# Kernel tuning notes

Hardware: AMD Instinct MI355X
Metric: run time of the kernel (lower is better)

The kernel has to match this reference:

```python
import jax, jax.numpy as jnp
import numpy as np
from jax.scipy.special import gammaln

ADIM, ODIM = 256, 80
B, T_TEXT, T_FEATS = 4, 160, 800


def conv1d(x, w, b, pad):
    # x: (B, C_in, T), w: (C_out, C_in, K)
    y = jax.lax.conv_general_dilated(x, w, (1,), [(pad, pad)],
                                     dimension_numbers=('NCH', 'OIH', 'NCH'))
    return y + b[None, :, None]


def betaln(x, y):
    return gammaln(x) + gammaln(y) - gammaln(x + y)


def beta_binomial_prior(T, N, w=1.0):
    # Matches scipy betabinom.logpmf(k, N, alpha, beta) with
    # alpha = w*arange(1, T+1), beta = w*(T - alpha + 1), k = arange(N).
    a = w * jnp.arange(1, T + 1, dtype=jnp.float32)          # (T,)
    b = w * (T - a + 1.0)                                    # (T,)
    k = jnp.arange(N, dtype=jnp.float32)[:, None]            # (N, 1)
    Nf = jnp.float32(N)
    logp = (gammaln(Nf + 1.0) - gammaln(k + 1.0) - gammaln(Nf - k + 1.0)
            + betaln(k + a, Nf - k + b) - betaln(a, b))      # (N, T)
    return logp.T                                            # (T_feats, T_text)


def setup_inputs() -> dict:
    key = jax.random.key(0)
    ks = jax.random.split(key, 12)
    s = 0.05
    return {
        'text': jax.random.normal(ks[0], (B, T_TEXT, ADIM), jnp.float32),
        'feats': jax.random.normal(ks[1], (B, T_FEATS, ODIM), jnp.float32),
        'text_lengths': jnp.full((B,), T_TEXT, dtype=jnp.int32),
        'feats_lengths': jnp.full((B,), T_FEATS, dtype=jnp.int32),
        'x_masks': jnp.zeros((B, T_TEXT), dtype=bool),
        't_w1': jax.random.normal(ks[2], (ADIM, ADIM, 3), jnp.float32) * s,
        't_b1': jnp.zeros((ADIM,), jnp.float32),
        't_w2': jax.random.normal(ks[3], (ADIM, ADIM, 1), jnp.float32) * s,
        't_b2': jnp.zeros((ADIM,), jnp.float32),
        'f_w1': jax.random.normal(ks[4], (ADIM, ODIM, 3), jnp.float32) * s,
        'f_b1': jnp.zeros((ADIM,), jnp.float32),
        'f_w2': jax.random.normal(ks[5], (ADIM, ADIM, 3), jnp.float32) * s,
        'f_b2': jnp.zeros((ADIM,), jnp.float32),
        'f_w3': jax.random.normal(ks[6], (ADIM, ADIM, 1), jnp.float32) * s,
        'f_b3': jnp.zeros((ADIM,), jnp.float32),
    }


def reference(text, feats, text_lengths, feats_lengths, x_masks,
              t_w1, t_b1, t_w2, t_b2, f_w1, f_b1, f_w2, f_b2, f_w3, f_b3):
    # text conv stem: (B, T_text, adim) -> (B, T_text, adim)
    t = jnp.swapaxes(text, 1, 2)
    t = jax.nn.relu(conv1d(t, t_w1, t_b1, 1))
    t = conv1d(t, t_w2, t_b2, 0)
    t = jnp.swapaxes(t, 1, 2)
    # feats conv stem: (B, T_feats, odim) -> (B, T_feats, adim)
    f = jnp.swapaxes(feats, 1, 2)
    f = jax.nn.relu(conv1d(f, f_w1, f_b1, 1))
    f = jax.nn.relu(conv1d(f, f_w2, f_b2, 1))
    f = conv1d(f, f_w3, f_b3, 0)
    f = jnp.swapaxes(f, 1, 2)
    # L2-distance score: (B, T_feats, T_text)
    diff = f[:, :, None, :] - t[:, None, :, :]               # (B,Tf,Tt,adim)
    score = -jnp.sqrt(jnp.sum(diff * diff, axis=-1))
    score = jnp.where(x_masks[:, None, :], -jnp.inf, score)
    log_p_attn = jax.nn.log_softmax(score, axis=-1)
    # beta-binomial prior (lengths == max, so prior fills the whole matrix)
    prior = beta_binomial_prior(feats.shape[1], text.shape[1])
    return log_p_attn + prior[None, :, :]
```

## Files before the change

### kernel.cpp

```cpp
#include <hip/hip_runtime.h>
#include <math.h>

#define NB 4
#define TTEXT 160
#define TFEAT 800

typedef __bf16 bf16x8 __attribute__((ext_vector_type(8)));
typedef float f32x4 __attribute__((ext_vector_type(4)));

__device__ inline unsigned short f2bf(float f) {
    unsigned int u = __builtin_bit_cast(unsigned int, f);
    unsigned int r = u + 0x7fffu + ((u >> 16) & 1u);
    return (unsigned short)(r >> 16);
}
__device__ inline float bf2f(unsigned short h) {
    unsigned int u = ((unsigned int)h) << 16;
    return __builtin_bit_cast(float, u);
}

__device__ inline float lgamma_int(float nf) {
    float z = nf, corr = 0.0f;
    if (nf < 8.0f) {
        const float p = nf * (nf + 1.0f) * (nf + 2.0f) * (nf + 3.0f)
                      * (nf + 4.0f) * (nf + 5.0f) * (nf + 6.0f) * (nf + 7.0f);
        z = nf + 8.0f;
        corr = logf(p);
    }
    const float lz = logf(z);
    const float iz = 1.0f / z;
    const float s = (z - 0.5f) * lz - z + 0.918938533f
                  + iz * (0.0833333333f - iz * iz * 0.00277777778f);
    return s - corr;
}

__global__ __launch_bounds__(256) void prep_kernel(
    const float* __restrict__ tw1, const float* __restrict__ tw2,
    const float* __restrict__ fw1, const float* __restrict__ fw2,
    const float* __restrict__ fw3,
    unsigned short* __restrict__ wb_t1, unsigned short* __restrict__ wb_t2,
    unsigned short* __restrict__ wb_f1, unsigned short* __restrict__ wb_f2,
    unsigned short* __restrict__ wb_f3)
{
    const int u = blockIdx.x * 256 + threadIdx.x;
    int rem = u;
    int CIN, CINP, K; const float* src; unsigned short* dst;
    if (rem < 196608)                  { CIN = 256; CINP = 256; K = 3; src = tw1; dst = wb_t1; }
    else if ((rem -= 196608) < 65536)  { CIN = 256; CINP = 256; K = 1; src = tw2; dst = wb_t2; }
    else if ((rem -= 65536) < 73728)   { CIN = 80;  CINP = 96;  K = 3; src = fw1; dst = wb_f1; }
    else if ((rem -= 73728) < 196608)  { CIN = 256; CINP = 256; K = 3; src = fw2; dst = wb_f2; }
    else { rem -= 196608;                CIN = 256; CINP = 256; K = 1; src = fw3; dst = wb_f3; }
    const int q = rem & 31, coc = rem >> 5, co = coc & 255, c = coc >> 8;
    const int cpk = CINP / 32, k = c / cpk, ci = (c % cpk) * 32 + q;
    const float v = (ci < CIN) ? src[((size_t)co * CIN + ci) * K + k] : 0.0f;
    dst[rem] = f2bf(v);
}

__global__ __launch_bounds__(1024) void stems_kernel(
    const float* __restrict__ text, const float* __restrict__ feats,
    const unsigned short* __restrict__ wt1, const float* __restrict__ bt1,
    const unsigned short* __restrict__ wt2, const float* __restrict__ bt2,
    const unsigned short* __restrict__ wf1, const float* __restrict__ bf1v,
    const unsigned short* __restrict__ wf2, const float* __restrict__ bf2v,
    const unsigned short* __restrict__ wf3, const float* __restrict__ bf3v,
    unsigned short* __restrict__ tB, float* __restrict__ tnorm,
    unsigned short* __restrict__ fC, float* __restrict__ fnorm)
{
    __shared__ __align__(16) unsigned short s[11056];
    __shared__ float s_red[16][16];
    const int tid = threadIdx.x;
    const int w  = tid >> 6;
    const int l  = tid & 63;
    const int lr = l & 15;
    const int lk = l >> 4;
    const int co0 = w * 16;
    const int koff = lk * 8;
    const int bid = blockIdx.x;

    if (bid < 40) {
        const int b  = bid & 3;
        const int t0 = (bid >> 2) << 4;
        unsigned short* s_in  = s;
        unsigned short* s_mid = s + 4752;

        for (int idx = tid; idx < 18 * 64; idx += 1024) {
            const int r = idx >> 6, c4 = idx & 63;
            const int x = t0 - 1 + r;
            float4 v = {0.f, 0.f, 0.f, 0.f};
            if (x >= 0 && x < TTEXT)
                v = *(const float4*)(text + ((size_t)(b * TTEXT + x)) * 256 + c4 * 4);
            unsigned short* p = s_in + r * 264 + c4 * 4;
            p[0] = f2bf(v.x); p[1] = f2bf(v.y); p[2] = f2bf(v.z); p[3] = f2bf(v.w);
        }
        __syncthreads();

        f32x4 acc = {0.f, 0.f, 0.f, 0.f};
#pragma unroll 8
        for (int c = 0; c < 24; ++c) {
            const int k  = c >> 3;
            const int ci = ((c & 7) << 5) + koff;
            const bf16x8 a = *(const bf16x8*)(s_in + (lr + k) * 264 + ci);
            const bf16x8 bb = *(const bf16x8*)(wt1 + (((size_t)c * 256 + co0 + lr) << 5) + koff);
            acc = __builtin_amdgcn_mfma_f32_16x16x32_bf16(a, bb, acc, 0, 0, 0);
        }
        {
            const float bv = bt1[co0 + lr];
#pragma unroll
            for (int r = 0; r < 4; ++r)
                s_mid[(lk * 4 + r) * 264 + co0 + lr] = f2bf(fmaxf(acc[r] + bv, 0.f));
        }
        __syncthreads();

        f32x4 a2 = {0.f, 0.f, 0.f, 0.f};
#pragma unroll
        for (int c = 0; c < 8; ++c) {
            const bf16x8 a = *(const bf16x8*)(s_mid + lr * 264 + (c << 5) + koff);
            const bf16x8 bb = *(const bf16x8*)(wt2 + (((size_t)c * 256 + co0 + lr) << 5) + koff);
            a2 = __builtin_amdgcn_mfma_f32_16x16x32_bf16(a, bb, a2, 0, 0, 0);
        }
        const float bv2 = bt2[co0 + lr];
#pragma unroll
        for (int r = 0; r < 4; ++r) {
            const int row = lk * 4 + r;
            const unsigned short h = f2bf(a2[r] + bv2);
            tB[((size_t)(b * TTEXT + t0 + row)) * 256 + co0 + lr] = h;
            const float vq = bf2f(h);
            float np = vq * vq;
            np += __shfl_xor(np, 1);
            np += __shfl_xor(np, 2);
            np += __shfl_xor(np, 4);
            np += __shfl_xor(np, 8);
            if (lr == 0) s_red[row][w] = np;
        }
        __syncthreads();
        if (tid < 16) {
            float s4 = 0.f;
#pragma unroll
            for (int ww = 0; ww < 16; ++ww) s4 += s_red[tid][ww];
            tnorm[b * TTEXT + t0 + tid] = s4;
        }
    } else {
        const int fb = bid - 40;
        const int b  = fb & 3;
        const int t0 = (fb >> 2) << 4;
        unsigned short* s_fin = s;
        unsigned short* s_b1  = s + 2080;
        unsigned short* s_b2  = s + 6832;

        for (int idx = tid; idx < 20 * 24; idx += 1024) {
            const int r  = idx / 24, c4 = idx - r * 24;
            const int ch = c4 * 4;
            const int x  = t0 - 2 + r;
            float4 v = {0.f, 0.f, 0.f, 0.f};
            if (ch < 80 && x >= 0 && x < TFEAT)
                v = *(const float4*)(feats + ((size_t)(b * TFEAT + x)) * 80 + ch);
            unsigned short* p = s_fin + r * 104 + ch;
            p[0] = f2bf(v.x); p[1] = f2bf(v.y); p[2] = f2bf(v.z); p[3] = f2bf(v.w);
        }
        __syncthreads();

        f32x4 acc1[2];
#pragma unroll
        for (int m = 0; m < 2; ++m) acc1[m] = {0.f, 0.f, 0.f, 0.f};
#pragma unroll
        for (int c = 0; c < 9; ++c) {
            const int k  = c / 3;
            const int ci = (c - k * 3) * 32 + koff;
            const bf16x8 bb = *(const bf16x8*)(wf1 + (((size_t)c * 256 + co0 + lr) << 5) + koff);
#pragma unroll
            for (int m = 0; m < 2; ++m) {
                int rr = m * 16 + lr + k;
                if (rr > 19) rr = 19;
                const bf16x8 a = *(const bf16x8*)(s_fin + rr * 104 + ci);
                acc1[m] = __builtin_amdgcn_mfma_f32_16x16x32_bf16(a, bb, acc1[m], 0, 0, 0);
            }
        }
        {
            const float bv = bf1v[co0 + lr];
#pragma unroll
            for (int m = 0; m < 2; ++m)
#pragma unroll
                for (int r = 0; r < 4; ++r) {
                    const int i = m * 16 + lk * 4 + r;
                    if (i < 18)
                        s_b1[i * 264 + co0 + lr] = f2bf(fmaxf(acc1[m][r] + bv, 0.f));
                }
        }
        __syncthreads();

        f32x4 acc2 = {0.f, 0.f, 0.f, 0.f};
#pragma unroll 8
        for (int c = 0; c < 24; ++c) {
            const int k  = c >> 3;
            const int ci = ((c & 7) << 5) + koff;
            const bf16x8 a = *(const bf16x8*)(s_b1 + (lr + k) * 264 + ci);
            const bf16x8 bb = *(const bf16x8*)(wf2 + (((size_t)c * 256 + co0 + lr) << 5) + koff);
            acc2 = __builtin_amdgcn_mfma_f32_16x16x32_bf16(a, bb, acc2, 0, 0, 0);
        }
        {
            const float bv = bf2v[co0 + lr];
#pragma unroll
            for (int r = 0; r < 4; ++r)
                s_b2[(lk * 4 + r) * 264 + co0 + lr] = f2bf(fmaxf(acc2[r] + bv, 0.f));
        }
        __syncthreads();

        f32x4 a3 = {0.f, 0.f, 0.f, 0.f};
#pragma unroll
        for (int c = 0; c < 8; ++c) {
            const bf16x8 a = *(const bf16x8*)(s_b2 + lr * 264 + (c << 5) + koff);
            const bf16x8 bb = *(const bf16x8*)(wf3 + (((size_t)c * 256 + co0 + lr) << 5) + koff);
            a3 = __builtin_amdgcn_mfma_f32_16x16x32_bf16(a, bb, a3, 0, 0, 0);
        }
        const float bv3 = bf3v[co0 + lr];
#pragma unroll
        for (int r = 0; r < 4; ++r) {
            const int row = lk * 4 + r;
            const unsigned short h = f2bf(a3[r] + bv3);
            fC[((size_t)(b * TFEAT + t0 + row)) * 256 + co0 + lr] = h;
            const float vq = bf2f(h);
            float np = vq * vq;
            np += __shfl_xor(np, 1);
            np += __shfl_xor(np, 2);
            np += __shfl_xor(np, 4);
            np += __shfl_xor(np, 8);
            if (lr == 0) s_red[row][w] = np;
        }
        __syncthreads();
        if (tid < 16) {
            float s4 = 0.f;
#pragma unroll
            for (int ww = 0; ww < 16; ++ww) s4 += s_red[tid][ww];
            fnorm[b * TFEAT + t0 + tid] = s4;
        }
    }
}

__global__ __launch_bounds__(512) void score_mfma(
    const unsigned short* __restrict__ F, const unsigned short* __restrict__ Tt,
    const float* __restrict__ fnorm, const float* __restrict__ tnorm,
    const unsigned char* __restrict__ xmask,
    float* __restrict__ out)
{
    const int b  = blockIdx.y;
    const int tid = threadIdx.x;
    const int w  = tid >> 6;
    const int l  = tid & 63;
    const int lr = l & 15;
    const int lk = l >> 4;
    const int i0 = blockIdx.x * 16;
    const int NI = (w < 2) ? 2 : 1;

    __shared__ float s_lg[962];
    __shared__ float s_red[16][8];
    __shared__ float s_red2[16][8];

    for (int idx = tid; idx < 962; idx += 512)
        s_lg[idx] = (idx >= 1) ? lgamma_int((float)idx) : 0.0f;

    f32x4 acc[2];
#pragma unroll
    for (int ni = 0; ni < 2; ++ni) acc[ni] = {0.f, 0.f, 0.f, 0.f};

    const unsigned short* __restrict__ Fp = F + ((size_t)(b * TFEAT + i0 + lr)) * 256;
    const unsigned short* __restrict__ Tp = Tt + ((size_t)b * TTEXT) * 256;

#pragma unroll
    for (int c = 0; c < 8; ++c) {
        const int d = c * 32 + lk * 8;
        const bf16x8 a = *(const bf16x8*)(Fp + d);
#pragma unroll
        for (int ni = 0; ni < 2; ++ni) {
            if (ni < NI) {
                const int n = w + ni * 8;
                const bf16x8 bb = *(const bf16x8*)(Tp + ((size_t)(n * 16 + lr)) * 256 + d);
                acc[ni] = __builtin_amdgcn_mfma_f32_16x16x32_bf16(a, bb, acc[ni], 0, 0, 0);
            }
        }
    }

    float fn[4];
#pragma unroll
    for (int r = 0; r < 4; ++r) fn[r] = fnorm[b * TFEAT + i0 + lk * 4 + r];
    float tn[2]; bool mk[2];
#pragma unroll
    for (int ni = 0; ni < 2; ++ni) {
        if (ni < NI) {
            const int j = (w + ni * 8) * 16 + lr;
            tn[ni] = tnorm[b * TTEXT + j];
            mk[ni] = xmask[b * TTEXT + j] != 0;
        } else { tn[ni] = 0.f; mk[ni] = true; }
    }
    float sc[2][4];
#pragma unroll
    for (int ni = 0; ni < 2; ++ni)
#pragma unroll
        for (int r = 0; r < 4; ++r) {
            const float d2 = fn[r] + tn[ni] - 2.0f * acc[ni][r];
            const float sv = -sqrtf(fmaxf(d2, 0.0f));
            sc[ni][r] = mk[ni] ? -INFINITY : sv;
        }

#pragma unroll
    for (int r = 0; r < 4; ++r) {
        float mx = fmaxf(sc[0][r], sc[1][r]);
        mx = fmaxf(mx, __shfl_xor(mx, 1));
        mx = fmaxf(mx, __shfl_xor(mx, 2));
        mx = fmaxf(mx, __shfl_xor(mx, 4));
        mx = fmaxf(mx, __shfl_xor(mx, 8));
        if (lr == 0) s_red[lk * 4 + r][w] = mx;
    }
    __syncthreads();
    float gmax[4];
#pragma unroll
    for (int r = 0; r < 4; ++r) {
        const int row = lk * 4 + r;
        float g = s_red[row][0];
#pragma unroll
        for (int ww = 1; ww < 8; ++ww) g = fmaxf(g, s_red[row][ww]);
        gmax[r] = g;
        float sm = 0.f;
#pragma unroll
        for (int ni = 0; ni < 2; ++ni)
            if (ni < NI) sm += expf(sc[ni][r] - g);
        sm += __shfl_xor(sm, 1);
        sm += __shfl_xor(sm, 2);
        sm += __shfl_xor(sm, 4);
        sm += __shfl_xor(sm, 8);
        if (lr == 0) s_red2[row][w] = sm;
    }
    __syncthreads();

    const float cst = s_lg[161] - s_lg[961] + s_lg[801];
#pragma unroll
    for (int r = 0; r < 4; ++r) {
        const int row = lk * 4 + r;
        float ssum = s_red2[row][0];
#pragma unroll
        for (int ww = 1; ww < 8; ++ww) ssum += s_red2[row][ww];
        const float lse = gmax[r] + logf(ssum);
        const int grow = i0 + row;
        const float rowterm = cst - s_lg[grow + 1] - s_lg[801 - grow];
#pragma unroll
        for (int ni = 0; ni < 2; ++ni) {
            if (ni < NI) {
                const int j = (w + ni * 8) * 16 + lr;
                const float prior = rowterm - s_lg[j + 1] - s_lg[160 - j]
                                  + s_lg[grow + j + 1] + s_lg[960 - grow - j];
                out[((size_t)(b * TFEAT + grow)) * TTEXT + j] = sc[ni][r] - lse + prior;
            }
        }
    }
}

extern "C" void kernel_launch(void* const* d_in, const int* in_sizes, int n_in,
                              void* d_out, int out_size, void* d_ws, size_t ws_size,
                              hipStream_t stream) {
    const float* text  = (const float*)d_in[0];
    const float* feats = (const float*)d_in[1];
    const unsigned char* xmask = (const unsigned char*)d_in[4];
    const float* t_w1 = (const float*)d_in[5];
    const float* t_b1 = (const float*)d_in[6];
    const float* t_w2 = (const float*)d_in[7];
    const float* t_b2 = (const float*)d_in[8];
    const float* f_w1 = (const float*)d_in[9];
    const float* f_b1 = (const float*)d_in[10];
    const float* f_w2 = (const float*)d_in[11];
    const float* f_b2 = (const float*)d_in[12];
    const float* f_w3 = (const float*)d_in[13];
    const float* f_b3 = (const float*)d_in[14];
    float* out = (float*)d_out;

    char* wp = (char*)d_ws;
    auto alloc = [&](size_t bytes) -> void* {
        void* p = wp; wp += (bytes + 255) & ~(size_t)255; return p;
    };
    unsigned short* wb_t1 = (unsigned short*)alloc(196608 * 2);
    unsigned short* wb_t2 = (unsigned short*)alloc(65536 * 2);
    unsigned short* wb_f1 = (unsigned short*)alloc(73728 * 2);
    unsigned short* wb_f2 = (unsigned short*)alloc(196608 * 2);
    unsigned short* wb_f3 = (unsigned short*)alloc(65536 * 2);
    unsigned short* tB = (unsigned short*)alloc((size_t)NB * TTEXT * 256 * 2);
    unsigned short* fC = (unsigned short*)alloc((size_t)NB * TFEAT * 256 * 2);
    float* fnorm = (float*)alloc((size_t)NB * TFEAT * 4);
    float* tnorm = (float*)alloc((size_t)NB * TTEXT * 4);

    prep_kernel<<<2336, 256, 0, stream>>>(
        t_w1, t_w2, f_w1, f_w2, f_w3, wb_t1, wb_t2, wb_f1, wb_f2, wb_f3);

    stems_kernel<<<240, 1024, 0, stream>>>(
        text, feats,
        wb_t1, t_b1, wb_t2, t_b2,
        wb_f1, f_b1, wb_f2, f_b2, wb_f3, f_b3,
        tB, tnorm, fC, fnorm);

    score_mfma<<<dim3(50, NB), 512, 0, stream>>>(fC, tB, fnorm, tnorm, xmask, out);
}
```

Before: 33.37 us.

## Merge text stem with weight prep and fuse feats stem into score kernel

Reduces three launches to two. The first kernel runs the text conv stem, reading fp32 weights directly and converting them to bf16 on the fly, while its extra blocks convert the feats weights to bf16. The second kernel runs the feats stem and keeps its output tile in shared memory, then computes distances, log-softmax and the prior in the same block. This removes the fC/fnorm round trip through global memory and one launch. In exchange it adds strided fp32 weight reads in the text stem, and only 10 of 16 waves are active in the score phase.

```diff
diff --git a/kernel.cpp b/kernel.cpp
--- a/kernel.cpp
+++ b/kernel.cpp
@@ -7,6 +7,7 @@
 
 typedef __bf16 bf16x8 __attribute__((ext_vector_type(8)));
 typedef float f32x4 __attribute__((ext_vector_type(4)));
+typedef unsigned short us8 __attribute__((ext_vector_type(8)));
 
 __device__ inline unsigned short f2bf(float f) {
     unsigned int u = __builtin_bit_cast(unsigned int, f);
@@ -33,40 +34,127 @@
     return s - corr;
 }
 
-__global__ __launch_bounds__(256) void prep_kernel(
-    const float* __restrict__ tw1, const float* __restrict__ tw2,
-    const float* __restrict__ fw1, const float* __restrict__ fw2,
-    const float* __restrict__ fw3,
-    unsigned short* __restrict__ wb_t1, unsigned short* __restrict__ wb_t2,
+__global__ __launch_bounds__(1024) void k1_text_prep(
+    const float* __restrict__ text,
+    const float* __restrict__ t_w1, const float* __restrict__ t_b1,
+    const float* __restrict__ t_w2, const float* __restrict__ t_b2,
+    const float* __restrict__ f_w1, const float* __restrict__ f_w2,
+    const float* __restrict__ f_w3,
     unsigned short* __restrict__ wb_f1, unsigned short* __restrict__ wb_f2,
-    unsigned short* __restrict__ wb_f3)
+    unsigned short* __restrict__ wb_f3,
+    unsigned short* __restrict__ tB, float* __restrict__ tnorm)
 {
-    const int u = blockIdx.x * 256 + threadIdx.x;
-    int rem = u;
-    int CIN, CINP, K; const float* src; unsigned short* dst;
-    if (rem < 196608)                  { CIN = 256; CINP = 256; K = 3; src = tw1; dst = wb_t1; }
-    else if ((rem -= 196608) < 65536)  { CIN = 256; CINP = 256; K = 1; src = tw2; dst = wb_t2; }
-    else if ((rem -= 65536) < 73728)   { CIN = 80;  CINP = 96;  K = 3; src = fw1; dst = wb_f1; }
-    else if ((rem -= 73728) < 196608)  { CIN = 256; CINP = 256; K = 3; src = fw2; dst = wb_f2; }
-    else { rem -= 196608;                CIN = 256; CINP = 256; K = 1; src = fw3; dst = wb_f3; }
-    const int q = rem & 31, coc = rem >> 5, co = coc & 255, c = coc >> 8;
-    const int cpk = CINP / 32, k = c / cpk, ci = (c % cpk) * 32 + q;
-    const float v = (ci < CIN) ? src[((size_t)co * CIN + ci) * K + k] : 0.0f;
-    dst[rem] = f2bf(v);
-}
-
-__global__ __launch_bounds__(1024) void stems_kernel(
-    const float* __restrict__ text, const float* __restrict__ feats,
-    const unsigned short* __restrict__ wt1, const float* __restrict__ bt1,
-    const unsigned short* __restrict__ wt2, const float* __restrict__ bt2,
+    const int bid = blockIdx.x;
+    const int tid = threadIdx.x;
+
+    if (bid >= 40) {
+        const int u = (bid - 40) * 1024 + tid;
+        int rem = u;
+        int CIN, CINP, K; const float* src; unsigned short* dst;
+        if (rem < 73728)                  { CIN = 80;  CINP = 96;  K = 3; src = f_w1; dst = wb_f1; }
+        else if ((rem -= 73728) < 196608) { CIN = 256; CINP = 256; K = 3; src = f_w2; dst = wb_f2; }
+        else { rem -= 196608;               CIN = 256; CINP = 256; K = 1; src = f_w3; dst = wb_f3; }
+        const int q = rem & 31, coc = rem >> 5, co = coc & 255, c = coc >> 8;
+        const int cpk = CINP / 32, k = c / cpk, ci = (c % cpk) * 32 + q;
+        const float v = (ci < CIN) ? src[((size_t)co * CIN + ci) * K + k] : 0.0f;
+        dst[rem] = f2bf(v);
+        return;
+    }
+
+    __shared__ __align__(16) unsigned short s[8976];
+    __shared__ float s_red[16][16];
+    const int w  = tid >> 6;
+    const int l  = tid & 63;
+    const int lr = l & 15;
+    const int lk = l >> 4;
+    const int co0 = w * 16;
+    const int koff = lk * 8;
+    const int b  = bid & 3;
+    const int t0 = (bid >> 2) << 4;
+    unsigned short* s_in  = s;
+    unsigned short* s_mid = s + 4752;
+
+    for (int idx = tid; idx < 18 * 64; idx += 1024) {
+        const int r = idx >> 6, c4 = idx & 63;
+        const int x = t0 - 1 + r;
+        float4 v = {0.f, 0.f, 0.f, 0.f};
+        if (x >= 0 && x < TTEXT)
+            v = *(const float4*)(text + ((size_t)(b * TTEXT + x)) * 256 + c4 * 4);
+        unsigned short* p = s_in + r * 264 + c4 * 4;
+        p[0] = f2bf(v.x); p[1] = f2bf(v.y); p[2] = f2bf(v.z); p[3] = f2bf(v.w);
+    }
+    __syncthreads();
+
+    f32x4 acc = {0.f, 0.f, 0.f, 0.f};
+#pragma unroll 4
+    for (int c = 0; c < 24; ++c) {
+        const int k  = c >> 3;
+        const int ci = ((c & 7) << 5) + koff;
+        const bf16x8 a = *(const bf16x8*)(s_in + (lr + k) * 264 + ci);
+        const float* wp = t_w1 + ((size_t)(co0 + lr) * 256 + ci) * 3 + k;
+        us8 hv;
+#pragma unroll
+        for (int j = 0; j < 8; ++j) hv[j] = f2bf(wp[j * 3]);
+        acc = __builtin_amdgcn_mfma_f32_16x16x32_bf16(
+            a, __builtin_bit_cast(bf16x8, hv), acc, 0, 0, 0);
+    }
+    {
+        const float bv = t_b1[co0 + lr];
+#pragma unroll
+        for (int r = 0; r < 4; ++r)
+            s_mid[(lk * 4 + r) * 264 + co0 + lr] = f2bf(fmaxf(acc[r] + bv, 0.f));
+    }
+    __syncthreads();
+
+    f32x4 a2 = {0.f, 0.f, 0.f, 0.f};
+#pragma unroll
+    for (int c = 0; c < 8; ++c) {
+        const bf16x8 a = *(const bf16x8*)(s_mid + lr * 264 + (c << 5) + koff);
+        const float* wp = t_w2 + (size_t)(co0 + lr) * 256 + (c << 5) + koff;
+        const float4 u0 = *(const float4*)wp;
+        const float4 u1 = *(const float4*)(wp + 4);
+        us8 hv;
+        hv[0] = f2bf(u0.x); hv[1] = f2bf(u0.y); hv[2] = f2bf(u0.z); hv[3] = f2bf(u0.w);
+        hv[4] = f2bf(u1.x); hv[5] = f2bf(u1.y); hv[6] = f2bf(u1.z); hv[7] = f2bf(u1.w);
+        a2 = __builtin_amdgcn_mfma_f32_16x16x32_bf16(
+            a, __builtin_bit_cast(bf16x8, hv), a2, 0, 0, 0);
+    }
+    const float bv2 = t_b2[co0 + lr];
+#pragma unroll
+    for (int r = 0; r < 4; ++r) {
+        const int row = lk * 4 + r;
+        const unsigned short h = f2bf(a2[r] + bv2);
+        tB[((size_t)(b * TTEXT + t0 + row)) * 256 + co0 + lr] = h;
+        const float vq = bf2f(h);
+        float np = vq * vq;
+        np += __shfl_xor(np, 1);
+        np += __shfl_xor(np, 2);
+        np += __shfl_xor(np, 4);
+        np += __shfl_xor(np, 8);
+        if (lr == 0) s_red[row][w] = np;
+    }
+    __syncthreads();
+    if (tid < 16) {
+        float s4 = 0.f;
+#pragma unroll
+        for (int ww = 0; ww < 16; ++ww) s4 += s_red[tid][ww];
+        tnorm[b * TTEXT + t0 + tid] = s4;
+    }
+}
+
+__global__ __launch_bounds__(1024) void k2_feats_score(
+    const float* __restrict__ feats, const unsigned char* __restrict__ xmask,
     const unsigned short* __restrict__ wf1, const float* __restrict__ bf1v,
     const unsigned short* __restrict__ wf2, const float* __restrict__ bf2v,
     const unsigned short* __restrict__ wf3, const float* __restrict__ bf3v,
-    unsigned short* __restrict__ tB, float* __restrict__ tnorm,
-    unsigned short* __restrict__ fC, float* __restrict__ fnorm)
+    const unsigned short* __restrict__ tB, const float* __restrict__ tnorm,
+    float* __restrict__ out)
 {
     __shared__ __align__(16) unsigned short s[11056];
     __shared__ float s_red[16][16];
+    __shared__ float s_red2[16][16];
+    __shared__ float s_fn[16];
+    __shared__ float s_lg[962];
     const int tid = threadIdx.x;
     const int w  = tid >> 6;
     const int l  = tid & 63;
@@ -74,235 +162,139 @@
     const int lk = l >> 4;
     const int co0 = w * 16;
     const int koff = lk * 8;
-    const int bid = blockIdx.x;
-
-    if (bid < 40) {
-        const int b  = bid & 3;
-        const int t0 = (bid >> 2) << 4;
-        unsigned short* s_in  = s;
-        unsigned short* s_mid = s + 4752;
-
-        for (int idx = tid; idx < 18 * 64; idx += 1024) {
-            const int r = idx >> 6, c4 = idx & 63;
-            const int x = t0 - 1 + r;
-            float4 v = {0.f, 0.f, 0.f, 0.f};
-            if (x >= 0 && x < TTEXT)
-                v = *(const float4*)(text + ((size_t)(b * TTEXT + x)) * 256 + c4 * 4);
-            unsigned short* p = s_in + r * 264 + c4 * 4;
-            p[0] = f2bf(v.x); p[1] = f2bf(v.y); p[2] = f2bf(v.z); p[3] = f2bf(v.w);
+    const int fb = blockIdx.x;
+    const int b  = fb & 3;
+    const int t0 = (fb >> 2) << 4;
+
+    unsigned short* s_fin = s;
+    unsigned short* s_b1  = s + 2080;
+    unsigned short* s_b2  = s + 6832;
+    unsigned short* s_out = s;
+
+    if (tid < 962) s_lg[tid] = (tid >= 1) ? lgamma_int((float)tid) : 0.0f;
+
+    for (int idx = tid; idx < 20 * 24; idx += 1024) {
+        const int r  = idx / 24, c4 = idx - r * 24;
+        const int ch = c4 * 4;
+        const int x  = t0 - 2 + r;
+        float4 v = {0.f, 0.f, 0.f, 0.f};
+        if (ch < 80 && x >= 0 && x < TFEAT)
+            v = *(const float4*)(feats + ((size_t)(b * TFEAT + x)) * 80 + ch);
+        unsigned short* p = s_fin + r * 104 + ch;
+        p[0] = f2bf(v.x); p[1] = f2bf(v.y); p[2] = f2bf(v.z); p[3] = f2bf(v.w);
+    }
+    __syncthreads();
+
+    f32x4 acc1[2];
+#pragma unroll
+    for (int m = 0; m < 2; ++m) acc1[m] = {0.f, 0.f, 0.f, 0.f};
+#pragma unroll
+    for (int c = 0; c < 9; ++c) {
+        const int k  = c / 3;
+        const int ci = (c - k * 3) * 32 + koff;
+        const bf16x8 bb = *(const bf16x8*)(wf1 + (((size_t)c * 256 + co0 + lr) << 5) + koff);
+#pragma unroll
+        for (int m = 0; m < 2; ++m) {
+            int rr = m * 16 + lr + k;
+            if (rr > 19) rr = 19;
+            const bf16x8 a = *(const bf16x8*)(s_fin + rr * 104 + ci);
+            acc1[m] = __builtin_amdgcn_mfma_f32_16x16x32_bf16(a, bb, acc1[m], 0, 0, 0);
         }
-        __syncthreads();
-
-        f32x4 acc = {0.f, 0.f, 0.f, 0.f};
+    }
+    {
+        const float bv = bf1v[co0 + lr];
+#pragma unroll
+        for (int m = 0; m < 2; ++m)
+#pragma unroll
+            for (int r = 0; r < 4; ++r) {
+                const int i = m * 16 + lk * 4 + r;
+                if (i < 18)
+                    s_b1[i * 264 + co0 + lr] = f2bf(fmaxf(acc1[m][r] + bv, 0.f));
+            }
+    }
+    __syncthreads();
+
+    f32x4 acc2 = {0.f, 0.f, 0.f, 0.f};
 #pragma unroll 8
-        for (int c = 0; c < 24; ++c) {
-            const int k  = c >> 3;
-            const int ci = ((c & 7) << 5) + koff;
-            const bf16x8 a = *(const bf16x8*)(s_in + (lr + k) * 264 + ci);
-            const bf16x8 bb = *(const bf16x8*)(wt1 + (((size_t)c * 256 + co0 + lr) << 5) + koff);
+    for (int c = 0; c < 24; ++c) {
+        const int k  = c >> 3;
+        const int ci = ((c & 7) << 5) + koff;
+        const bf16x8 a = *(const bf16x8*)(s_b1 + (lr + k) * 264 + ci);
+        const bf16x8 bb = *(const bf16x8*)(wf2 + (((size_t)c * 256 + co0 + lr) << 5) + koff);
+        acc2 = __builtin_amdgcn_mfma_f32_16x16x32_bf16(a, bb, acc2, 0, 0, 0);
+    }
+    {
+        const float bv = bf2v[co0 + lr];
+#pragma unroll
+        for (int r = 0; r < 4; ++r)
+            s_b2[(lk * 4 + r) * 264 + co0 + lr] = f2bf(fmaxf(acc2[r] + bv, 0.f));
+    }
+    __syncthreads();
+
+    f32x4 a3 = {0.f, 0.f, 0.f, 0.f};
+#pragma unroll
+    for (int c = 0; c < 8; ++c) {
+        const bf16x8 a = *(const bf16x8*)(s_b2 + lr * 264 + (c << 5) + koff);
+        const bf16x8 bb = *(const bf16x8*)(wf3 + (((size_t)c * 256 + co0 + lr) << 5) + koff);
+        a3 = __builtin_amdgcn_mfma_f32_16x16x32_bf16(a, bb, a3, 0, 0, 0);
+    }
+    const float bv3 = bf3v[co0 + lr];
+#pragma unroll
+    for (int r = 0; r < 4; ++r) {
+        const int row = lk * 4 + r;
+        const unsigned short h = f2bf(a3[r] + bv3);
+        s_out[row * 264 + co0 + lr] = h;
+        const float vq = bf2f(h);
+        float np = vq * vq;
+        np += __shfl_xor(np, 1);
+        np += __shfl_xor(np, 2);
+        np += __shfl_xor(np, 4);
+        np += __shfl_xor(np, 8);
+        if (lr == 0) s_red[row][w] = np;
+    }
+    __syncthreads();
+    if (tid < 16) {
+        float s4 = 0.f;
+#pragma unroll
+        for (int ww = 0; ww < 16; ++ww) s4 += s_red[tid][ww];
+        s_fn[tid] = s4;
+    }
+    __syncthreads();
+
+    const bool act = (w < 10);
+    f32x4 acc = {0.f, 0.f, 0.f, 0.f};
+    const unsigned short* __restrict__ Tp = tB + ((size_t)b * TTEXT) * 256;
+
+#pragma unroll
+    for (int c = 0; c < 8; ++c) {
+        const int d = c * 32 + koff;
+        const bf16x8 a = *(const bf16x8*)(s_out + lr * 264 + d);
+        if (act) {
+            const bf16x8 bb = *(const bf16x8*)(Tp + ((size_t)(w * 16 + lr)) * 256 + d);
             acc = __builtin_amdgcn_mfma_f32_16x16x32_bf16(a, bb, acc, 0, 0, 0);
         }
-        {
-            const float bv = bt1[co0 + lr];
-#pragma unroll
-            for (int r = 0; r < 4; ++r)
-                s_mid[(lk * 4 + r) * 264 + co0 + lr] = f2bf(fmaxf(acc[r] + bv, 0.f));
-        }
-        __syncthreads();
-
-        f32x4 a2 = {0.f, 0.f, 0.f, 0.f};
-#pragma unroll
-        for (int c = 0; c < 8; ++c) {
-            const bf16x8 a = *(const bf16x8*)(s_mid + lr * 264 + (c << 5) + koff);
-            const bf16x8 bb = *(const bf16x8*)(wt2 + (((size_t)c * 256 + co0 + lr) << 5) + koff);
-            a2 = __builtin_amdgcn_mfma_f32_16x16x32_bf16(a, bb, a2, 0, 0, 0);
-        }
-        const float bv2 = bt2[co0 + lr];
-#pragma unroll
-        for (int r = 0; r < 4; ++r) {
-            const int row = lk * 4 + r;
-            const unsigned short h = f2bf(a2[r] + bv2);
-            tB[((size_t)(b * TTEXT + t0 + row)) * 256 + co0 + lr] = h;
-            const float vq = bf2f(h);
-            float np = vq * vq;
-            np += __shfl_xor(np, 1);
-            np += __shfl_xor(np, 2);
-            np += __shfl_xor(np, 4);
-            np += __shfl_xor(np, 8);
-            if (lr == 0) s_red[row][w] = np;
-        }
-        __syncthreads();
-        if (tid < 16) {
-            float s4 = 0.f;
-#pragma unroll
-            for (int ww = 0; ww < 16; ++ww) s4 += s_red[tid][ww];
-            tnorm[b * TTEXT + t0 + tid] = s4;
-        }
-    } else {
-        const int fb = bid - 40;
-        const int b  = fb & 3;
-        const int t0 = (fb >> 2) << 4;
-        unsigned short* s_fin = s;
-        unsigned short* s_b1  = s + 2080;
-        unsigned short* s_b2  = s + 6832;
-
-        for (int idx = tid; idx < 20 * 24; idx += 1024) {
-            const int r  = idx / 24, c4 = idx - r * 24;
-            const int ch = c4 * 4;
-            const int x  = t0 - 2 + r;
-            float4 v = {0.f, 0.f, 0.f, 0.f};
-            if (ch < 80 && x >= 0 && x < TFEAT)
-                v = *(const float4*)(feats + ((size_t)(b * TFEAT + x)) * 80 + ch);
-            unsigned short* p = s_fin + r * 104 + ch;
-            p[0] = f2bf(v.x); p[1] = f2bf(v.y); p[2] = f2bf(v.z); p[3] = f2bf(v.w);
-        }
-        __syncthreads();
-
-        f32x4 acc1[2];
-#pragma unroll
-        for (int m = 0; m < 2; ++m) acc1[m] = {0.f, 0.f, 0.f, 0.f};
-#pragma unroll
-        for (int c = 0; c < 9; ++c) {
-            const int k  = c / 3;
-            const int ci = (c - k * 3) * 32 + koff;
-            const bf16x8 bb = *(const bf16x8*)(wf1 + (((size_t)c * 256 + co0 + lr) << 5) + koff);
-#pragma unroll
-            for (int m = 0; m < 2; ++m) {
-                int rr = m * 16 + lr + k;
-                if (rr > 19) rr = 19;
-                const bf16x8 a = *(const bf16x8*)(s_fin + rr * 104 + ci);
-                acc1[m] = __builtin_amdgcn_mfma_f32_16x16x32_bf16(a, bb, acc1[m], 0, 0, 0);
-            }
-        }
-        {
-            const float bv = bf1v[co0 + lr];
-#pragma unroll
-            for (int m = 0; m < 2; ++m)
-#pragma unroll
-                for (int r = 0; r < 4; ++r) {
-                    const int i = m * 16 + lk * 4 + r;
-                    if (i < 18)
-                        s_b1[i * 264 + co0 + lr] = f2bf(fmaxf(acc1[m][r] + bv, 0.f));
-                }
-        }
-        __syncthreads();
-
-        f32x4 acc2 = {0.f, 0.f, 0.f, 0.f};
-#pragma unroll 8
-        for (int c = 0; c < 24; ++c) {
-            const int k  = c >> 3;
-            const int ci = ((c & 7) << 5) + koff;
-            const bf16x8 a = *(const bf16x8*)(s_b1 + (lr + k) * 264 + ci);
-            const bf16x8 bb = *(const bf16x8*)(wf2 + (((size_t)c * 256 + co0 + lr) << 5) + koff);
-            acc2 = __builtin_amdgcn_mfma_f32_16x16x32_bf16(a, bb, acc2, 0, 0, 0);
-        }
-        {
-            const float bv = bf2v[co0 + lr];
-#pragma unroll
-            for (int r = 0; r < 4; ++r)
-                s_b2[(lk * 4 + r) * 264 + co0 + lr] = f2bf(fmaxf(acc2[r] + bv, 0.f));
-        }
-        __syncthreads();
-
-        f32x4 a3 = {0.f, 0.f, 0.f, 0.f};
-#pragma unroll
-        for (int c = 0; c < 8; ++c) {
-            const bf16x8 a = *(const bf16x8*)(s_b2 + lr * 264 + (c << 5) + koff);
-            const bf16x8 bb = *(const bf16x8*)(wf3 + (((size_t)c * 256 + co0 + lr) << 5) + koff);
-            a3 = __builtin_amdgcn_mfma_f32_16x16x32_bf16(a, bb, a3, 0, 0, 0);
-        }
-        const float bv3 = bf3v[co0 + lr];
-#pragma unroll
-        for (int r = 0; r < 4; ++r) {
-            const int row = lk * 4 + r;
-            const unsigned short h = f2bf(a3[r] + bv3);
-            fC[((size_t)(b * TFEAT + t0 + row)) * 256 + co0 + lr] = h;
-            const float vq = bf2f(h);
-            float np = vq * vq;
-            np += __shfl_xor(np, 1);
-            np += __shfl_xor(np, 2);
-            np += __shfl_xor(np, 4);
-            np += __shfl_xor(np, 8);
-            if (lr == 0) s_red[row][w] = np;
-        }
-        __syncthreads();
-        if (tid < 16) {
-            float s4 = 0.f;
-#pragma unroll
-            for (int ww = 0; ww < 16; ++ww) s4 += s_red[tid][ww];
-            fnorm[b * TFEAT + t0 + tid] = s4;
-        }
-    }
-}
-
-__global__ __launch_bounds__(512) void score_mfma(
-    const unsigned short* __restrict__ F, const unsigned short* __restrict__ Tt,
-    const float* __restrict__ fnorm, const float* __restrict__ tnorm,
-    const unsigned char* __restrict__ xmask,
-    float* __restrict__ out)
-{
-    const int b  = blockIdx.y;
-    const int tid = threadIdx.x;
-    const int w  = tid >> 6;
-    const int l  = tid & 63;
-    const int lr = l & 15;
-    const int lk = l >> 4;
-    const int i0 = blockIdx.x * 16;
-    const int NI = (w < 2) ? 2 : 1;
-
-    __shared__ float s_lg[962];
-    __shared__ float s_red[16][8];
-    __shared__ float s_red2[16][8];
-
-    for (int idx = tid; idx < 962; idx += 512)
-        s_lg[idx] = (idx >= 1) ? lgamma_int((float)idx) : 0.0f;
-
-    f32x4 acc[2];
-#pragma unroll
-    for (int ni = 0; ni < 2; ++ni) acc[ni] = {0.f, 0.f, 0.f, 0.f};
-
-    const unsigned short* __restrict__ Fp = F + ((size_t)(b * TFEAT + i0 + lr)) * 256;
-    const unsigned short* __restrict__ Tp = Tt + ((size_t)b * TTEXT) * 256;
-
-#pragma unroll
-    for (int c = 0; c < 8; ++c) {
-        const int d = c * 32 + lk * 8;
-        const bf16x8 a = *(const bf16x8*)(Fp + d);
-#pragma unroll
-        for (int ni = 0; ni < 2; ++ni) {
-            if (ni < NI) {
-                const int n = w + ni * 8;
-                const bf16x8 bb = *(const bf16x8*)(Tp + ((size_t)(n * 16 + lr)) * 256 + d);
-                acc[ni] = __builtin_amdgcn_mfma_f32_16x16x32_bf16(a, bb, acc[ni], 0, 0, 0);
-            }
-        }
     }
 
     float fn[4];
 #pragma unroll
-    for (int r = 0; r < 4; ++r) fn[r] = fnorm[b * TFEAT + i0 + lk * 4 + r];
-    float tn[2]; bool mk[2];
-#pragma unroll
-    for (int ni = 0; ni < 2; ++ni) {
-        if (ni < NI) {
-            const int j = (w + ni * 8) * 16 + lr;
-            tn[ni] = tnorm[b * TTEXT + j];
-            mk[ni] = xmask[b * TTEXT + j] != 0;
-        } else { tn[ni] = 0.f; mk[ni] = true; }
-    }
-    float sc[2][4];
-#pragma unroll
-    for (int ni = 0; ni < 2; ++ni)
-#pragma unroll
-        for (int r = 0; r < 4; ++r) {
-            const float d2 = fn[r] + tn[ni] - 2.0f * acc[ni][r];
-            const float sv = -sqrtf(fmaxf(d2, 0.0f));
-            sc[ni][r] = mk[ni] ? -INFINITY : sv;
-        }
-
-#pragma unroll
-    for (int r = 0; r < 4; ++r) {
-        float mx = fmaxf(sc[0][r], sc[1][r]);
+    for (int r = 0; r < 4; ++r) fn[r] = s_fn[lk * 4 + r];
+    float tn = 0.f; bool mk = true;
+    if (act) {
+        const int j = w * 16 + lr;
+        tn = tnorm[b * TTEXT + j];
+        mk = xmask[b * TTEXT + j] != 0;
+    }
+    float sc[4];
+#pragma unroll
+    for (int r = 0; r < 4; ++r) {
+        const float d2 = fn[r] + tn - 2.0f * acc[r];
+        const float sv = -sqrtf(fmaxf(d2, 0.0f));
+        sc[r] = mk ? -INFINITY : sv;
+    }
+
+#pragma unroll
+    for (int r = 0; r < 4; ++r) {
+        float mx = sc[r];
         mx = fmaxf(mx, __shfl_xor(mx, 1));
         mx = fmaxf(mx, __shfl_xor(mx, 2));
         mx = fmaxf(mx, __shfl_xor(mx, 4));
@@ -316,12 +308,9 @@
         const int row = lk * 4 + r;
         float g = s_red[row][0];
 #pragma unroll
-        for (int ww = 1; ww < 8; ++ww) g = fmaxf(g, s_red[row][ww]);
+        for (int ww = 1; ww < 16; ++ww) g = fmaxf(g, s_red[row][ww]);
         gmax[r] = g;
-        float sm = 0.f;
-#pragma unroll
-        for (int ni = 0; ni < 2; ++ni)
-            if (ni < NI) sm += expf(sc[ni][r] - g);
+        float sm = act ? expf(sc[r] - g) : 0.0f;
         sm += __shfl_xor(sm, 1);
         sm += __shfl_xor(sm, 2);
         sm += __shfl_xor(sm, 4);
@@ -336,18 +325,15 @@
         const int row = lk * 4 + r;
         float ssum = s_red2[row][0];
 #pragma unroll
-        for (int ww = 1; ww < 8; ++ww) ssum += s_red2[row][ww];
+        for (int ww = 1; ww < 16; ++ww) ssum += s_red2[row][ww];
         const float lse = gmax[r] + logf(ssum);
-        const int grow = i0 + row;
+        const int grow = t0 + row;
         const float rowterm = cst - s_lg[grow + 1] - s_lg[801 - grow];
-#pragma unroll
-        for (int ni = 0; ni < 2; ++ni) {
-            if (ni < NI) {
-                const int j = (w + ni * 8) * 16 + lr;
-                const float prior = rowterm - s_lg[j + 1] - s_lg[160 - j]
-                                  + s_lg[grow + j + 1] + s_lg[960 - grow - j];
-                out[((size_t)(b * TFEAT + grow)) * TTEXT + j] = sc[ni][r] - lse + prior;
-            }
+        if (act) {
+            const int j = w * 16 + lr;
+            const float prior = rowterm - s_lg[j + 1] - s_lg[160 - j]
+                              + s_lg[grow + j + 1] + s_lg[960 - grow - j];
+            out[((size_t)(b * TFEAT + grow)) * TTEXT + j] = sc[r] - lse + prior;
         }
     }
 }
@@ -374,24 +360,17 @@
     auto alloc = [&](size_t bytes) -> void* {
         void* p = wp; wp += (bytes + 255) & ~(size_t)255; return p;
     };
-    unsigned short* wb_t1 = (unsigned short*)alloc(196608 * 2);
-    unsigned short* wb_t2 = (unsigned short*)alloc(65536 * 2);
     unsigned short* wb_f1 = (unsigned short*)alloc(73728 * 2);
     unsigned short* wb_f2 = (unsigned short*)alloc(196608 * 2);
     unsigned short* wb_f3 = (unsigned short*)alloc(65536 * 2);
     unsigned short* tB = (unsigned short*)alloc((size_t)NB * TTEXT * 256 * 2);
-    unsigned short* fC = (unsigned short*)alloc((size_t)NB * TFEAT * 256 * 2);
-    float* fnorm = (float*)alloc((size_t)NB * TFEAT * 4);
     float* tnorm = (float*)alloc((size_t)NB * TTEXT * 4);
 
-    prep_kernel<<<2336, 256, 0, stream>>>(
-        t_w1, t_w2, f_w1, f_w2, f_w3, wb_t1, wb_t2, wb_f1, wb_f2, wb_f3);
-
-    stems_kernel<<<240, 1024, 0, stream>>>(
-        text, feats,
-        wb_t1, t_b1, wb_t2, t_b2,
-        wb_f1, f_b1, wb_f2, f_b2, wb_f3, f_b3,
-        tB, tnorm, fC, fnorm);
-
-    score_mfma<<<dim3(50, NB), 512, 0, stream>>>(fC, tB, fnorm, tnorm, xmask, out);
-}
+    k1_text_prep<<<368, 1024, 0, stream>>>(
+        text, t_w1, t_b1, t_w2, t_b2, f_w1, f_w2, f_w3,
+        wb_f1, wb_f2, wb_f3, tB, tnorm);
+
+    k2_feats_score<<<200, 1024, 0, stream>>>(
+        feats, xmask, wb_f1, f_b1, wb_f2, f_b2, wb_f3, f_b3,
+        tB, tnorm, out);
+}
```

Result: slower. 117.5 us (+252.2%).

## Replicate bf16 weights per XCD so stem blocks read XCD-local copies

Applied to the files above, without the earlier changes.

The prep kernel now writes eight copies of the converted bf16 conv weights, one per XCD, and each stem block selects its copy using the hardware XCD id read from a register. The goal is for each XCD's L2 to hold its own copy, so that cross-die traffic and contention on one shared weight buffer are avoided. In exchange, prep launches eight times as many blocks and writes eight times as much data, which adds time to that stage.

```diff
diff --git a/kernel.cpp b/kernel.cpp
--- a/kernel.cpp
+++ b/kernel.cpp
@@ -4,6 +4,13 @@
 #define NB 4
 #define TTEXT 160
 #define TFEAT 800
+
+#define OFF_T1 0
+#define OFF_T2 196608
+#define OFF_F1 262144
+#define OFF_F2 335872
+#define OFF_F3 532480
+#define REP_ELEMS 598016
 
 typedef __bf16 bf16x8 __attribute__((ext_vector_type(8)));
 typedef float f32x4 __attribute__((ext_vector_type(4)));
@@ -33,35 +40,37 @@
     return s - corr;
 }
 
+__device__ inline unsigned xcd_id() {
+    return __builtin_amdgcn_s_getreg(63508) & 7u;
+}
+
 __global__ __launch_bounds__(256) void prep_kernel(
     const float* __restrict__ tw1, const float* __restrict__ tw2,
     const float* __restrict__ fw1, const float* __restrict__ fw2,
     const float* __restrict__ fw3,
-    unsigned short* __restrict__ wb_t1, unsigned short* __restrict__ wb_t2,
-    unsigned short* __restrict__ wb_f1, unsigned short* __restrict__ wb_f2,
-    unsigned short* __restrict__ wb_f3)
+    unsigned short* __restrict__ wb_all)
 {
-    const int u = blockIdx.x * 256 + threadIdx.x;
+    const int rep = blockIdx.x & 7;
+    const int u = (blockIdx.x >> 3) * 256 + threadIdx.x;
     int rem = u;
-    int CIN, CINP, K; const float* src; unsigned short* dst;
-    if (rem < 196608)                  { CIN = 256; CINP = 256; K = 3; src = tw1; dst = wb_t1; }
-    else if ((rem -= 196608) < 65536)  { CIN = 256; CINP = 256; K = 1; src = tw2; dst = wb_t2; }
-    else if ((rem -= 65536) < 73728)   { CIN = 80;  CINP = 96;  K = 3; src = fw1; dst = wb_f1; }
-    else if ((rem -= 73728) < 196608)  { CIN = 256; CINP = 256; K = 3; src = fw2; dst = wb_f2; }
-    else { rem -= 196608;                CIN = 256; CINP = 256; K = 1; src = fw3; dst = wb_f3; }
+    int CIN, CINP, K; const float* src; int off;
+    if (rem < 196608)                  { CIN = 256; CINP = 256; K = 3; src = tw1; off = OFF_T1; }
+    else if ((rem -= 196608) < 65536)  { CIN = 256; CINP = 256; K = 1; src = tw2; off = OFF_T2; }
+    else if ((rem -= 65536) < 73728)   { CIN = 80;  CINP = 96;  K = 3; src = fw1; off = OFF_F1; }
+    else if ((rem -= 73728) < 196608)  { CIN = 256; CINP = 256; K = 3; src = fw2; off = OFF_F2; }
+    else { rem -= 196608;                CIN = 256; CINP = 256; K = 1; src = fw3; off = OFF_F3; }
     const int q = rem & 31, coc = rem >> 5, co = coc & 255, c = coc >> 8;
     const int cpk = CINP / 32, k = c / cpk, ci = (c % cpk) * 32 + q;
     const float v = (ci < CIN) ? src[((size_t)co * CIN + ci) * K + k] : 0.0f;
-    dst[rem] = f2bf(v);
+    wb_all[(size_t)rep * REP_ELEMS + off + rem] = f2bf(v);
 }
 
 __global__ __launch_bounds__(1024) void stems_kernel(
     const float* __restrict__ text, const float* __restrict__ feats,
-    const unsigned short* __restrict__ wt1, const float* __restrict__ bt1,
-    const unsigned short* __restrict__ wt2, const float* __restrict__ bt2,
-    const unsigned short* __restrict__ wf1, const float* __restrict__ bf1v,
-    const unsigned short* __restrict__ wf2, const float* __restrict__ bf2v,
-    const unsigned short* __restrict__ wf3, const float* __restrict__ bf3v,
+    const unsigned short* __restrict__ wb_all,
+    const float* __restrict__ bt1, const float* __restrict__ bt2,
+    const float* __restrict__ bf1v, const float* __restrict__ bf2v,
+    const float* __restrict__ bf3v,
     unsigned short* __restrict__ tB, float* __restrict__ tnorm,
     unsigned short* __restrict__ fC, float* __restrict__ fnorm)
 {
@@ -75,6 +84,13 @@
     const int co0 = w * 16;
     const int koff = lk * 8;
     const int bid = blockIdx.x;
+
+    const unsigned short* __restrict__ wbase = wb_all + (size_t)xcd_id() * REP_ELEMS;
+    const unsigned short* __restrict__ wt1 = wbase + OFF_T1;
+    const unsigned short* __restrict__ wt2 = wbase + OFF_T2;
+    const unsigned short* __restrict__ wf1 = wbase + OFF_F1;
+    const unsigned short* __restrict__ wf2 = wbase + OFF_F2;
+    const unsigned short* __restrict__ wf3 = wbase + OFF_F3;
 
     if (bid < 40) {
         const int b  = bid & 3;
@@ -374,23 +390,18 @@
     auto alloc = [&](size_t bytes) -> void* {
         void* p = wp; wp += (bytes + 255) & ~(size_t)255; return p;
     };
-    unsigned short* wb_t1 = (unsigned short*)alloc(196608 * 2);
-    unsigned short* wb_t2 = (unsigned short*)alloc(65536 * 2);
-    unsigned short* wb_f1 = (unsigned short*)alloc(73728 * 2);
-    unsigned short* wb_f2 = (unsigned short*)alloc(196608 * 2);
-    unsigned short* wb_f3 = (unsigned short*)alloc(65536 * 2);
+    unsigned short* wb_all = (unsigned short*)alloc((size_t)8 * REP_ELEMS * 2);
     unsigned short* tB = (unsigned short*)alloc((size_t)NB * TTEXT * 256 * 2);
     unsigned short* fC = (unsigned short*)alloc((size_t)NB * TFEAT * 256 * 2);
     float* fnorm = (float*)alloc((size_t)NB * TFEAT * 4);
     float* tnorm = (float*)alloc((size_t)NB * TTEXT * 4);
 
-    prep_kernel<<<2336, 256, 0, stream>>>(
-        t_w1, t_w2, f_w1, f_w2, f_w3, wb_t1, wb_t2, wb_f1, wb_f2, wb_f3);
+    prep_kernel<<<2336 * 8, 256, 0, stream>>>(
+        t_w1, t_w2, f_w1, f_w2, f_w3, wb_all);
 
     stems_kernel<<<240, 1024, 0, stream>>>(
-        text, feats,
-        wb_t1, t_b1, wb_t2, t_b2,
-        wb_f1, f_b1, wb_f2, f_b2, wb_f3, f_b3,
+        text, feats, wb_all,
+        t_b1, t_b2, f_b1, f_b2, f_b3,
         tB, tnorm, fC, fnorm);
 
     score_mfma<<<dim3(50, NB), 512, 0, stream>>>(fC, tB, fnorm, tnorm, xmask, out);
```

Result: slower. 38.09 us (+14.1%).

## Stage conv weights into LDS via async global_load_lds triple-buffer pipeline

Applied to the files above, without the earlier changes.

Weight fragments for every conv stage are now prefetched two chunks ahead into three LDS buffers with global_load_lds, using vmcnt waits, and read from LDS instead of directly from global memory. The aim is to hide global-memory latency on the weight stream behind the MFMA work. Each wave stages only its own slice, so no barrier is needed. It adds 48KB of LDS per block, which may limit occupancy, and relies on manual vmcnt counting.

```diff
diff --git a/kernel.cpp b/kernel.cpp
--- a/kernel.cpp
+++ b/kernel.cpp
@@ -32,6 +32,19 @@
                   + iz * (0.0833333333f - iz * iz * 0.00277777778f);
     return s - corr;
 }
+
+__device__ __forceinline__ void gll16(const unsigned short* g, unsigned short* l) {
+    __builtin_amdgcn_global_load_lds(
+        (const __attribute__((address_space(1))) void*)g,
+        (__attribute__((address_space(3))) void*)l, 16, 0, 0);
+}
+__device__ __forceinline__ unsigned short* bufsel(
+    unsigned short* a, unsigned short* b, unsigned short* c_, int i) {
+    return (i == 0) ? a : (i == 1) ? b : c_;
+}
+
+#define STAGE(W, c, buf) gll16((W) + ((size_t)(c) << 13) + (w << 9) + (l << 3), (buf) + (w << 9))
+#define WAITV(n) asm volatile("s_waitcnt vmcnt(" #n ")" ::: "memory")
 
 __global__ __launch_bounds__(256) void prep_kernel(
     const float* __restrict__ tw1, const float* __restrict__ tw2,
@@ -66,6 +79,9 @@
     unsigned short* __restrict__ fC, float* __restrict__ fnorm)
 {
     __shared__ __align__(16) unsigned short s[11056];
+    __shared__ __align__(16) unsigned short ws0[8192];
+    __shared__ __align__(16) unsigned short ws1[8192];
+    __shared__ __align__(16) unsigned short ws2[8192];
     __shared__ float s_red[16][16];
     const int tid = threadIdx.x;
     const int w  = tid >> 6;
@@ -94,12 +110,20 @@
         __syncthreads();
 
         f32x4 acc = {0.f, 0.f, 0.f, 0.f};
-#pragma unroll 8
+        STAGE(wt1, 0, ws0);
+        STAGE(wt1, 1, ws1);
+#pragma unroll 3
         for (int c = 0; c < 24; ++c) {
+            unsigned short* cur = bufsel(ws0, ws1, ws2, c % 3);
+            if (c < 22) {
+                unsigned short* nxt = bufsel(ws0, ws1, ws2, (c + 2) % 3);
+                STAGE(wt1, c + 2, nxt);
+                WAITV(2);
+            } else if (c == 22) { WAITV(1); } else { WAITV(0); }
             const int k  = c >> 3;
             const int ci = ((c & 7) << 5) + koff;
             const bf16x8 a = *(const bf16x8*)(s_in + (lr + k) * 264 + ci);
-            const bf16x8 bb = *(const bf16x8*)(wt1 + (((size_t)c * 256 + co0 + lr) << 5) + koff);
+            const bf16x8 bb = *(const bf16x8*)(cur + (w << 9) + lr * 32 + lk * 8);
             acc = __builtin_amdgcn_mfma_f32_16x16x32_bf16(a, bb, acc, 0, 0, 0);
         }
         {
@@ -111,10 +135,18 @@
         __syncthreads();
 
         f32x4 a2 = {0.f, 0.f, 0.f, 0.f};
+        STAGE(wt2, 0, ws0);
+        STAGE(wt2, 1, ws1);
 #pragma unroll
         for (int c = 0; c < 8; ++c) {
+            unsigned short* cur = bufsel(ws0, ws1, ws2, c % 3);
+            if (c < 6) {
+                unsigned short* nxt = bufsel(ws0, ws1, ws2, (c + 2) % 3);
+                STAGE(wt2, c + 2, nxt);
+                WAITV(2);
+            } else if (c == 6) { WAITV(1); } else { WAITV(0); }
             const bf16x8 a = *(const bf16x8*)(s_mid + lr * 264 + (c << 5) + koff);
-            const bf16x8 bb = *(const bf16x8*)(wt2 + (((size_t)c * 256 + co0 + lr) << 5) + koff);
+            const bf16x8 bb = *(const bf16x8*)(cur + (w << 9) + lr * 32 + lk * 8);
             a2 = __builtin_amdgcn_mfma_f32_16x16x32_bf16(a, bb, a2, 0, 0, 0);
         }
         const float bv2 = bt2[co0 + lr];
@@ -161,11 +193,19 @@
         f32x4 acc1[2];
 #pragma unroll
         for (int m = 0; m < 2; ++m) acc1[m] = {0.f, 0.f, 0.f, 0.f};
+        STAGE(wf1, 0, ws0);
+        STAGE(wf1, 1, ws1);
 #pragma unroll
         for (int c = 0; c < 9; ++c) {
+            unsigned short* cur = bufsel(ws0, ws1, ws2, c % 3);
+            if (c < 7) {
+                unsigned short* nxt = bufsel(ws0, ws1, ws2, (c + 2) % 3);
+                STAGE(wf1, c + 2, nxt);
+                WAITV(2);
+            } else if (c == 7) { WAITV(1); } else { WAITV(0); }
             const int k  = c / 3;
             const int ci = (c - k * 3) * 32 + koff;
-            const bf16x8 bb = *(const bf16x8*)(wf1 + (((size_t)c * 256 + co0 + lr) << 5) + koff);
+            const bf16x8 bb = *(const bf16x8*)(cur + (w << 9) + lr * 32 + lk * 8);
 #pragma unroll
             for (int m = 0; m < 2; ++m) {
                 int rr = m * 16 + lr + k;
@@ -188,12 +228,20 @@
         __syncthreads();
 
         f32x4 acc2 = {0.f, 0.f, 0.f, 0.f};
-#pragma unroll 8
+        STAGE(wf2, 0, ws0);
+        STAGE(wf2, 1, ws1);
+#pragma unroll 3
         for (int c = 0; c < 24; ++c) {
+            unsigned short* cur = bufsel(ws0, ws1, ws2, c % 3);
+            if (c < 22) {
+                unsigned short* nxt = bufsel(ws0, ws1, ws2, (c + 2) % 3);
+                STAGE(wf2, c + 2, nxt);
+                WAITV(2);
+            } else if (c == 22) { WAITV(1); } else { WAITV(0); }
             const int k  = c >> 3;
             const int ci = ((c & 7) << 5) + koff;
             const bf16x8 a = *(const bf16x8*)(s_b1 + (lr + k) * 264 + ci);
-            const bf16x8 bb = *(const bf16x8*)(wf2 + (((size_t)c * 256 + co0 + lr) << 5) + koff);
+            const bf16x8 bb = *(const bf16x8*)(cur + (w << 9) + lr * 32 + lk * 8);
             acc2 = __builtin_amdgcn_mfma_f32_16x16x32_bf16(a, bb, acc2, 0, 0, 0);
         }
         {
@@ -205,10 +253,18 @@
         __syncthreads();
 
         f32x4 a3 = {0.f, 0.f, 0.f, 0.f};
+        STAGE(wf3, 0, ws0);
+        STAGE(wf3, 1, ws1);
 #pragma unroll
         for (int c = 0; c < 8; ++c) {
+            unsigned short* cur = bufsel(ws0, ws1, ws2, c % 3);
+            if (c < 6) {
+                unsigned short* nxt = bufsel(ws0, ws1, ws2, (c + 2) % 3);
+                STAGE(wf3, c + 2, nxt);
+                WAITV(2);
+            } else if (c == 6) { WAITV(1); } else { WAITV(0); }
             const bf16x8 a = *(const bf16x8*)(s_b2 + lr * 264 + (c << 5) + koff);
-            const bf16x8 bb = *(const bf16x8*)(wf3 + (((size_t)c * 256 + co0 + lr) << 5) + koff);
+            const bf16x8 bb = *(const bf16x8*)(cur + (w << 9) + lr * 32 + lk * 8);
             a3 = __builtin_amdgcn_mfma_f32_16x16x32_bf16(a, bb, a3, 0, 0, 0);
         }
         const float bv3 = bf3v[co0 + lr];
```

Result: faster. 31.98 us (-4.2%).
